# Optimization experiments

Hardware: AMD Instinct MI355X
Metric: run time of the kernel (lower is better)

Reference implementation:

```python
import jax, jax.numpy as jnp
import numpy as np

GRID_EXTENT = 80.0  # world coords in [0, 80) per the t[0]*(W/80.0) mapping


def setup_inputs() -> dict:
    key = jax.random.key(0)
    k1, k2 = jax.random.split(key)
    B, C, H, W, N = 16, 8, 512, 512, 64
    preds = jax.random.normal(k1, (B, C, H, W), dtype=jnp.float32)
    # targets: (B, N, 7); coords t[...,0], t[...,1] in [0, 80)
    targets = jax.random.uniform(k2, (B, N, 7), dtype=jnp.float32) * GRID_EXTENT
    return {"preds": preds, "targets": targets}


def _build_maps(targets, B, H, W):
    # grid indices: int(clamp(t * (W/80), 0, W-1)) -- truncation == floor for nonneg
    gx = jnp.clip(targets[..., 0] * (W / GRID_EXTENT), 0, W - 1).astype(jnp.int32)  # (B,N)
    gy = jnp.clip(targets[..., 1] * (H / GRID_EXTENT), 0, H - 1).astype(jnp.int32)  # (B,N)
    b = jnp.broadcast_to(jnp.arange(B)[:, None], gx.shape)                           # (B,N)
    # vectorized scatter replacing the per-target Python loop
    tm = jnp.zeros((B, H, W, 7), targets.dtype).at[b, gy, gx].set(targets)  # (B,H,W,7)
    mask = jnp.zeros((B, H, W), targets.dtype).at[b, gy, gx].set(1.0)       # (B,H,W)
    return jnp.transpose(tm, (0, 3, 1, 2)), mask  # (B,7,H,W), (B,H,W)


def reference(preds, targets):
    B, _, H, W = preds.shape
    cls_preds = preds[:, 0]    # (B,H,W) logits
    reg_preds = preds[:, 1:]   # (B,7,H,W)
    target_map, mask = _build_maps(targets, B, H, W)

    # BCEWithLogitsLoss(reduction='mean'), numerically stable form
    x, z = cls_preds, mask
    cls_loss = jnp.mean(jnp.maximum(x, 0.0) - x * z + jnp.log1p(jnp.exp(-jnp.abs(x))))

    num_objects = mask.sum()

    # SmoothL1 (beta=1), reduction='none', masked mean over positive cells
    d = reg_preds - target_map
    ad = jnp.abs(d)
    sl1 = jnp.where(ad < 1.0, 0.5 * d * d, ad - 0.5)
    reg_loss = (sl1 * mask[:, None, :, :]).sum() / (num_objects + 1e-6)
    reg_loss = jnp.where(num_objects > 0, reg_loss, 0.0)

    total_loss = cls_loss + 2.0 * reg_loss
    return total_loss, num_objects
```

## Files before the change

### kernel.cpp

```cpp
#include <hip/hip_runtime.h>

#define B_   16
#define HW_  (512 * 512)
#define BHW  (B_ * HW_)
#define SCALE (512.0f / 80.0f)

#define NB1  1024
#define BLK  256


__device__ __forceinline__ float block_reduce_sum(float v, float* smem) {
    #pragma unroll
    for (int off = 32; off > 0; off >>= 1) v += __shfl_down(v, off);
    int lane = threadIdx.x & 63, wid = threadIdx.x >> 6;
    if (lane == 0) smem[wid] = v;
    __syncthreads();
    if (wid == 0) {
        v = (lane < (BLK >> 6)) ? smem[lane] : 0.0f;
        #pragma unroll
        for (int off = 32; off > 0; off >>= 1) v += __shfl_down(v, off);
    }
    return v;
}

__global__ __launch_bounds__(BLK) void det_main(
        const float* __restrict__ preds,
        const float* __restrict__ targets,
        float* __restrict__ ws) {
    __shared__ float smem[BLK / 64];

    if (blockIdx.x < NB1) {
        const float4* p4 = (const float4*)preds;
        const int tid = blockIdx.x * BLK + threadIdx.x;
        float local = 0.0f;
        #pragma unroll
        for (int k = 0; k < 4; ++k) {
            int i   = tid + k * (NB1 * BLK);
            int b   = i >> 16;
            int rem = i & 0xFFFF;
            float4 v = p4[((size_t)b << 19) + rem];
            local += fmaxf(v.x, 0.0f) + __logf(1.0f + __expf(-fabsf(v.x)));
            local += fmaxf(v.y, 0.0f) + __logf(1.0f + __expf(-fabsf(v.y)));
            local += fmaxf(v.z, 0.0f) + __logf(1.0f + __expf(-fabsf(v.z)));
            local += fmaxf(v.w, 0.0f) + __logf(1.0f + __expf(-fabsf(v.w)));
        }
        float s = block_reduce_sum(local, smem);
        if (threadIdx.x == 0) ws[blockIdx.x] = s;
        return;
    }

    __shared__ int cell[64];
    const int b = blockIdx.x - NB1;
    const int n = threadIdx.x & 63;
    const int g = threadIdx.x >> 6;
    const int t = (b << 6) + n;

    if (g == 0) {
        float tx = targets[t * 7 + 0];
        float ty = targets[t * 7 + 1];
        int gx = (int)fminf(fmaxf(tx * SCALE, 0.0f), 511.0f);
        int gy = (int)fminf(fmaxf(ty * SCALE, 0.0f), 511.0f);
        cell[n] = gy * 512 + gx;
    }
    __syncthreads();

    int c = cell[n];
    bool win = true;
    for (int n2 = n + 1; n2 < 64; ++n2) {
        if (cell[n2] == c) { win = false; break; }
    }

    float sum_x = 0.0f, reg = 0.0f, nobj = 0.0f;
    if (win) {
        size_t base = ((size_t)b << 21) + (size_t)c;
        if (g == 0) nobj = 1.0f;
        #pragma unroll
        for (int j = 0; j < 2; ++j) {
            int L = 2 * g + j;
            float p = preds[base + ((size_t)L << 18)];
            if (L == 0) {
                sum_x = p;
            } else {
                float d  = p - targets[t * 7 + (L - 1)];
                float ad = fabsf(d);
                reg += (ad < 1.0f) ? 0.5f * d * d : ad - 0.5f;
            }
        }
    }

    float rs = block_reduce_sum(sum_x, smem);
    __syncthreads();
    float rr = block_reduce_sum(reg, smem);
    __syncthreads();
    float rn = block_reduce_sum(nobj, smem);
    if (threadIdx.x == 0) {
        ws[NB1 + b * 3 + 0] = rs;
        ws[NB1 + b * 3 + 1] = rr;
        ws[NB1 + b * 3 + 2] = rn;
    }
}

__global__ __launch_bounds__(BLK) void det_finalize(
        const float* __restrict__ ws,
        float* __restrict__ out) {
    __shared__ float smem[BLK / 64];
    const float4* w4 = (const float4*)ws;
    float4 v = w4[threadIdx.x];
    float ps = v.x + v.y + v.z + v.w;

    float sx = 0.0f, rg = 0.0f, nb = 0.0f;
    if (threadIdx.x < 16) {
        sx = ws[NB1 + threadIdx.x * 3 + 0];
        rg = ws[NB1 + threadIdx.x * 3 + 1];
        nb = ws[NB1 + threadIdx.x * 3 + 2];
    }

    float rps = block_reduce_sum(ps, smem);
    __syncthreads();
    float rs = block_reduce_sum(sx, smem);
    __syncthreads();
    float rr = block_reduce_sum(rg, smem);
    __syncthreads();
    float rn = block_reduce_sum(nb, smem);

    if (threadIdx.x == 0) {
        float cls = (rps - rs) / (float)BHW;
        float rl  = (rn > 0.0f) ? rr / (rn + 1e-6f) : 0.0f;
        out[0] = cls + 2.0f * rl;
        out[1] = rn;
    }
}

extern "C" void kernel_launch(void* const* d_in, const int* in_sizes, int n_in,
                              void* d_out, int out_size, void* d_ws, size_t ws_size,
                              hipStream_t stream) {
    const float* preds   = (const float*)d_in[0];
    const float* targets = (const float*)d_in[1];
    float* out = (float*)d_out;
    float* ws  = (float*)d_ws;

    det_main<<<NB1 + B_, BLK, 0, stream>>>(preds, targets, ws);
    det_finalize<<<1, BLK, 0, stream>>>(ws, out);
}
```

Baseline: 171.0 us.

## Halve grid size, schedule target blocks first, fuse block reductions into float4

Cuts the streaming-block count to 512, so each thread now loads eight float4s instead of four. The 16 target-gather blocks move to the front of the grid so their latency-bound work starts early. The three separate block reductions, in both the main and finalize kernels, become one float4 shuffle reduction, which removes extra barriers. Fewer blocks can reduce occupancy and memory-level parallelism on a large-CU GPU.

```diff
diff --git a/kernel.cpp b/kernel.cpp
--- a/kernel.cpp
+++ b/kernel.cpp
@@ -5,20 +5,31 @@
 #define BHW  (B_ * HW_)
 #define SCALE (512.0f / 80.0f)
 
-#define NB1  1024
+#define NB1  512
+#define NTB  16
 #define BLK  256
 
 
-__device__ __forceinline__ float block_reduce_sum(float v, float* smem) {
+__device__ __forceinline__ float4 block_reduce_sum4(float4 v, float4* smem) {
     #pragma unroll
-    for (int off = 32; off > 0; off >>= 1) v += __shfl_down(v, off);
+    for (int off = 32; off > 0; off >>= 1) {
+        v.x += __shfl_down(v.x, off);
+        v.y += __shfl_down(v.y, off);
+        v.z += __shfl_down(v.z, off);
+        v.w += __shfl_down(v.w, off);
+    }
     int lane = threadIdx.x & 63, wid = threadIdx.x >> 6;
     if (lane == 0) smem[wid] = v;
     __syncthreads();
     if (wid == 0) {
-        v = (lane < (BLK >> 6)) ? smem[lane] : 0.0f;
+        v = (lane < (BLK >> 6)) ? smem[lane] : make_float4(0.f, 0.f, 0.f, 0.f);
         #pragma unroll
-        for (int off = 32; off > 0; off >>= 1) v += __shfl_down(v, off);
+        for (int off = 2; off > 0; off >>= 1) {
+            v.x += __shfl_down(v.x, off);
+            v.y += __shfl_down(v.y, off);
+            v.z += __shfl_down(v.z, off);
+            v.w += __shfl_down(v.w, off);
+        }
     }
     return v;
 }
@@ -27,14 +38,14 @@
         const float* __restrict__ preds,
         const float* __restrict__ targets,
         float* __restrict__ ws) {
-    __shared__ float smem[BLK / 64];
+    __shared__ float4 smem[BLK / 64];
 
-    if (blockIdx.x < NB1) {
+    if (blockIdx.x >= NTB) {
         const float4* p4 = (const float4*)preds;
-        const int tid = blockIdx.x * BLK + threadIdx.x;
+        const int tid = (blockIdx.x - NTB) * BLK + threadIdx.x;
         float local = 0.0f;
         #pragma unroll
-        for (int k = 0; k < 4; ++k) {
+        for (int k = 0; k < 8; ++k) {
             int i   = tid + k * (NB1 * BLK);
             int b   = i >> 16;
             int rem = i & 0xFFFF;
@@ -44,13 +55,13 @@
             local += fmaxf(v.z, 0.0f) + __logf(1.0f + __expf(-fabsf(v.z)));
             local += fmaxf(v.w, 0.0f) + __logf(1.0f + __expf(-fabsf(v.w)));
         }
-        float s = block_reduce_sum(local, smem);
-        if (threadIdx.x == 0) ws[blockIdx.x] = s;
+        float4 s = block_reduce_sum4(make_float4(local, 0.f, 0.f, 0.f), smem);
+        if (threadIdx.x == 0) ws[blockIdx.x - NTB] = s.x;
         return;
     }
 
     __shared__ int cell[64];
-    const int b = blockIdx.x - NB1;
+    const int b = blockIdx.x;
     const int n = threadIdx.x & 63;
     const int g = threadIdx.x >> 6;
     const int t = (b << 6) + n;
@@ -88,26 +99,24 @@
         }
     }
 
-    float rs = block_reduce_sum(sum_x, smem);
-    __syncthreads();
-    float rr = block_reduce_sum(reg, smem);
-    __syncthreads();
-    float rn = block_reduce_sum(nobj, smem);
+    float4 r = block_reduce_sum4(make_float4(sum_x, reg, nobj, 0.f), smem);
     if (threadIdx.x == 0) {
-        ws[NB1 + b * 3 + 0] = rs;
-        ws[NB1 + b * 3 + 1] = rr;
-        ws[NB1 + b * 3 + 2] = rn;
+        ws[NB1 + b * 3 + 0] = r.x;
+        ws[NB1 + b * 3 + 1] = r.y;
+        ws[NB1 + b * 3 + 2] = r.z;
     }
 }
 
 __global__ __launch_bounds__(BLK) void det_finalize(
         const float* __restrict__ ws,
         float* __restrict__ out) {
-    __shared__ float smem[BLK / 64];
-    const float4* w4 = (const float4*)ws;
-    float4 v = w4[threadIdx.x];
-    float ps = v.x + v.y + v.z + v.w;
+    __shared__ float4 smem[BLK / 64];
 
+    float ps = 0.0f;
+    if (threadIdx.x < NB1 / 4) {
+        float4 v = ((const float4*)ws)[threadIdx.x];
+        ps = v.x + v.y + v.z + v.w;
+    }
     float sx = 0.0f, rg = 0.0f, nb = 0.0f;
     if (threadIdx.x < 16) {
         sx = ws[NB1 + threadIdx.x * 3 + 0];
@@ -115,19 +124,13 @@
         nb = ws[NB1 + threadIdx.x * 3 + 2];
     }
 
-    float rps = block_reduce_sum(ps, smem);
-    __syncthreads();
-    float rs = block_reduce_sum(sx, smem);
-    __syncthreads();
-    float rr = block_reduce_sum(rg, smem);
-    __syncthreads();
-    float rn = block_reduce_sum(nb, smem);
+    float4 r = block_reduce_sum4(make_float4(ps, sx, rg, nb), smem);
 
     if (threadIdx.x == 0) {
-        float cls = (rps - rs) / (float)BHW;
-        float rl  = (rn > 0.0f) ? rr / (rn + 1e-6f) : 0.0f;
+        float cls = (r.x - r.y) / (float)BHW;
+        float rl  = (r.w > 0.0f) ? r.z / (r.w + 1e-6f) : 0.0f;
         out[0] = cls + 2.0f * rl;
-        out[1] = rn;
+        out[1] = r.w;
     }
 }
 
@@ -139,6 +142,6 @@
     float* out = (float*)d_out;
     float* ws  = (float*)d_ws;
 
-    det_main<<<NB1 + B_, BLK, 0, stream>>>(preds, targets, ws);
+    det_main<<<NTB + NB1, BLK, 0, stream>>>(preds, targets, ws);
     det_finalize<<<1, BLK, 0, stream>>>(ws, out);
 }
```

Result: faster. 165.7 us (-3.1%).
